# Kernel optimization log

Hardware: AMD Instinct MI355X
Metric: run time of the kernel (lower is better)

## Reference

```python
import jax, jax.numpy as jnp
import numpy as np


def _edge_softmax_by_src(e, src, n_nodes):
    # DGL edge_softmax(norm_by='src'): softmax over outgoing edges of each src node
    m = jax.ops.segment_max(e, src, num_segments=n_nodes)
    ex = jnp.exp(e - m[src])
    s = jax.ops.segment_sum(ex, src, num_segments=n_nodes)
    return ex / s[src]


def _l2norm(x):
    # F.normalize(p=2, dim=-1), eps=1e-12
    n = jnp.linalg.norm(x, axis=-1, keepdims=True)
    return x / jnp.maximum(n, 1e-12)


def setup_inputs() -> dict:
    key = jax.random.key(0)
    ks = jax.random.split(key, 16)
    N, E, D, NC = 50000, 1600000, 64, 16   # main graph nodes/edges, dim, classes
    NCL, ECL, FCL = 32, 1024, 16           # coarsened line graph: nodes=etypes
    s = 0.1
    inp = {
        "cl_h": jax.random.normal(ks[0], (NCL, FCL), jnp.float32),
        "cl_w": jax.random.normal(ks[1], (ECL,), jnp.float32),
        "cl_src": jax.random.randint(ks[2], (ECL,), 0, NCL, jnp.int32),
        "cl_dst": jax.random.randint(ks[3], (ECL,), 0, NCL, jnp.int32),
        "g_src": jax.random.randint(ks[4], (E,), 0, N, jnp.int32),
        "g_dst": jax.random.randint(ks[5], (E,), 0, N, jnp.int32),
        "g_etype": jax.random.randint(ks[6], (E,), 0, NCL, jnp.int32),
        # learned parameters
        "feats_emb": jax.random.normal(ks[7], (N, D), jnp.float32) * s,
        "W_e": jax.random.normal(ks[8], (FCL, D), jnp.float32) * s,      # linear_e (no bias)
        "beta1": jnp.array(1.0, jnp.float32),
        "eps1": jnp.array(0.0, jnp.float32),
        "beta2": jnp.array(1.0, jnp.float32),
        "eps2": jnp.array(0.0, jnp.float32),
        "W1a": jax.random.normal(ks[9], (D, D), jnp.float32) * s,
        "W2a": jax.random.normal(ks[10], (D, D), jnp.float32) * s,
        "W1b": jax.random.normal(ks[11], (D, D), jnp.float32) * s,
        "W2b": jax.random.normal(ks[12], (D, D), jnp.float32) * s,
        "W_pred": jax.random.normal(ks[13], (D, NC), jnp.float32) * s,
        "b_pred": jnp.zeros((NC,), jnp.float32),
    }
    return inp


def reference(cl_h, cl_w, cl_src, cl_dst, g_src, g_dst, g_etype,
              feats_emb, W_e, beta1, eps1, beta2, eps2,
              W1a, W2a, W1b, W2b, W_pred, b_pred):
    NCL = cl_h.shape[0]
    N = feats_emb.shape[0]

    def agnn(feat, beta, eps):
        p = _edge_softmax_by_src(beta * cl_w, cl_src, NCL)           # [Ecl]
        nh = _l2norm(feat)                                           # [NCL, F]
        agg = jax.ops.segment_sum(nh[cl_src] * p[:, None], cl_dst,
                                  num_segments=NCL)                  # [NCL, F]
        return (1.0 + eps) * feat + agg

    # edge-type feature propagation on coarsened line graph (dropout is eval-mode identity)
    h = jax.nn.relu(agnn(cl_h, beta1, eps1))
    h = jax.nn.relu(agnn(h, beta2, eps2))

    # per-edge relation embedding on main graph
    ew = h[g_etype] @ W_e                                            # [E, D]

    def gconv(feat, W1, W2):
        msg = feat[g_src] - ew                                       # u_sub_e, [E, D]
        agg = jax.ops.segment_sum(msg, g_dst, num_segments=N)        # [N, D]
        return jnp.tanh(feat @ W1 + agg @ W2)

    x = gconv(feats_emb, W1a, W2a)
    x = gconv(x, W1b, W2b)
    return x @ W_pred + b_pred
```

## Files before the change

### kernel.cpp

```cpp
#include <hip/hip_runtime.h>


#define TILE 8192

typedef __attribute__((ext_vector_type(8))) unsigned short us8;

__device__ __forceinline__ float b2f(unsigned short h) {
    return __uint_as_float(((unsigned)h) << 16);
}
__device__ __forceinline__ unsigned short f2b(float f) {
    const unsigned u = __float_as_uint(f);
    return (unsigned short)((u + 0x7FFFu + ((u >> 16) & 1u)) >> 16);
}

__device__ __forceinline__ unsigned ford_enc(float v) {
    unsigned b = __float_as_uint(v);
    return (b & 0x80000000u) ? ~b : (b | 0x80000000u);
}
__device__ __forceinline__ float ford_dec(unsigned k) {
    return __uint_as_float((k & 0x80000000u) ? (k ^ 0x80000000u) : ~k);
}

__global__ __launch_bounds__(512) void agnn_kernel(
    const float* __restrict__ cl_h, const float* __restrict__ cl_w,
    const int* __restrict__ cl_src, const int* __restrict__ cl_dst,
    const float* __restrict__ W_e,
    const float* __restrict__ pb1, const float* __restrict__ pe1,
    const float* __restrict__ pb2, const float* __restrict__ pe2,
    float* __restrict__ hW, int ECL)
{
    __shared__ float w_s[1024];
    __shared__ int   src_s[1024];
    __shared__ int   dst_s[1024];
    __shared__ float h[32][16];
    __shared__ float nh[32][16];
    __shared__ float p[1024];
    __shared__ float red[32][16];
    __shared__ float acc16[32][16][16];
    __shared__ unsigned mI[32];
    __shared__ float m[32], ssum[32], nrm[32];
    const int tid = threadIdx.x;
    const int seg = tid >> 4, j = tid & 15;

    for (int e = tid; e < ECL; e += 512) {
        w_s[e] = cl_w[e]; src_s[e] = cl_src[e]; dst_s[e] = cl_dst[e];
    }
    h[tid >> 4][tid & 15] = cl_h[tid];
    __syncthreads();

    for (int layer = 0; layer < 2; ++layer) {
        const float beta = layer ? *pb2 : *pb1;
        const float eps  = layer ? *pe2 : *pe1;

        if (tid < 32) mI[tid] = ford_enc(-3.4e38f);
        __syncthreads();
        for (int e = tid; e < ECL; e += 512)
            atomicMax(&mI[src_s[e]], ford_enc(beta * w_s[e]));
        __syncthreads();
        if (tid < 32) m[tid] = ford_dec(mI[tid]);
        __syncthreads();

        for (int e = tid; e < ECL; e += 512)
            p[e] = __expf(beta * w_s[e] - m[src_s[e]]);
        __syncthreads();

        {
            float s = 0.f;
            #pragma unroll 4
            for (int e = j; e < ECL; e += 16)
                s += (src_s[e] == seg) ? p[e] : 0.f;
            red[seg][j] = s;
        }
        __syncthreads();
        if (tid < 32) {
            float s = 0.f;
            #pragma unroll
            for (int k = 0; k < 16; ++k) s += red[tid][k];
            ssum[tid] = s;
            float q = 0.f;
            #pragma unroll
            for (int f = 0; f < 16; ++f) { float v = h[tid][f]; q += v * v; }
            nrm[tid] = fmaxf(sqrtf(q), 1e-12f);
        }
        __syncthreads();
        for (int e = tid; e < ECL; e += 512)
            p[e] = p[e] / ssum[src_s[e]];
        nh[tid >> 4][tid & 15] = h[tid >> 4][tid & 15] / nrm[tid >> 4];
        __syncthreads();

        {
            float facc[16];
            #pragma unroll
            for (int f = 0; f < 16; ++f) facc[f] = 0.f;
            #pragma unroll 4
            for (int e = j; e < ECL; e += 16) {
                if (dst_s[e] == seg) {
                    const float pe = p[e];
                    const float4* nhrow = reinterpret_cast<const float4*>(&nh[src_s[e]][0]);
                    const float4 a0 = nhrow[0], a1 = nhrow[1], a2 = nhrow[2], a3 = nhrow[3];
                    facc[0] += pe * a0.x; facc[1] += pe * a0.y; facc[2] += pe * a0.z; facc[3] += pe * a0.w;
                    facc[4] += pe * a1.x; facc[5] += pe * a1.y; facc[6] += pe * a1.z; facc[7] += pe * a1.w;
                    facc[8] += pe * a2.x; facc[9] += pe * a2.y; facc[10] += pe * a2.z; facc[11] += pe * a2.w;
                    facc[12] += pe * a3.x; facc[13] += pe * a3.y; facc[14] += pe * a3.z; facc[15] += pe * a3.w;
                }
            }
            #pragma unroll
            for (int f = 0; f < 16; ++f) acc16[seg][j][f] = facc[f];
        }
        __syncthreads();
        {
            const int t = tid >> 4, f = tid & 15;
            float a = 0.f;
            #pragma unroll
            for (int k = 0; k < 16; ++k) a += acc16[t][k][f];
            float v = (1.f + eps) * h[t][f] + a;
            h[t][f] = fmaxf(v, 0.f);
        }
        __syncthreads();
    }

    for (int o = tid; o < 2048; o += 512) {
        const int t = o >> 6, d = o & 63;
        float s = 0.f;
        #pragma unroll
        for (int f = 0; f < 16; ++f) s += h[t][f] * W_e[f * 64 + d];
        hW[o] = s;
    }
}

__global__ __launch_bounds__(256) void tobf16_kernel(
    const float* __restrict__ x, unsigned short* __restrict__ y, int total8)
{
    const int i = blockIdx.x * 256 + threadIdx.x;
    if (i >= total8) return;
    const int base = i * 8;
    const float4 a = *reinterpret_cast<const float4*>(&x[base]);
    const float4 b = *reinterpret_cast<const float4*>(&x[base + 4]);
    us8 o;
    o[0] = f2b(a.x); o[1] = f2b(a.y); o[2] = f2b(a.z); o[3] = f2b(a.w);
    o[4] = f2b(b.x); o[5] = f2b(b.y); o[6] = f2b(b.z); o[7] = f2b(b.w);
    *reinterpret_cast<us8*>(&y[base]) = o;
}

__global__ __launch_bounds__(256) void bucket_count(
    const int* __restrict__ dst, int* __restrict__ bcnt, int E)
{
    __shared__ int lh[256];
    const int tid = threadIdx.x;
    lh[tid] = 0;
    __syncthreads();
    const int base = blockIdx.x * TILE;
    #pragma unroll
    for (int it = 0; it < 8; ++it) {
        const int i = base + (it * 256 + tid) * 4;
        if (i + 3 < E) {
            const int4 d = *reinterpret_cast<const int4*>(&dst[i]);
            atomicAdd(&lh[d.x >> 8], 1); atomicAdd(&lh[d.y >> 8], 1);
            atomicAdd(&lh[d.z >> 8], 1); atomicAdd(&lh[d.w >> 8], 1);
        } else {
            for (int k = i; k < E && k < i + 4; ++k) atomicAdd(&lh[dst[k] >> 8], 1);
        }
    }
    __syncthreads();
    if (lh[tid]) atomicAdd(&bcnt[tid], lh[tid]);
}

__global__ __launch_bounds__(256) void bucket_scan(
    const int* __restrict__ bcnt, int* __restrict__ bbase, int* __restrict__ bcur)
{
    __shared__ int ws[4];
    const int tid = threadIdx.x, lane = tid & 63, wv = tid >> 6;
    const int v = bcnt[tid];
    int x = v;
    #pragma unroll
    for (int s = 1; s < 64; s <<= 1) { const int t = __shfl_up(x, s, 64); if (lane >= s) x += t; }
    if (lane == 63) ws[wv] = x;
    __syncthreads();
    if (tid == 0) { int a = ws[0]; ws[0] = 0; for (int k = 1; k < 4; ++k) { const int b = ws[k]; ws[k] = a; a += b; } }
    __syncthreads();
    const int excl = ws[wv] + x - v;
    bbase[tid] = excl; bcur[tid] = excl;
    if (tid == 255) bbase[256] = excl + v;
}

__global__ __launch_bounds__(256) void bucket_scatter(
    const int* __restrict__ src, const int* __restrict__ dst, const int* __restrict__ et,
    int* __restrict__ bcur, unsigned* __restrict__ etmp, int E)
{
    __shared__ int lh[256], lofs[256], lcur[256], gbase[256];
    __shared__ int ws[4];
    __shared__ unsigned stage[TILE];
    __shared__ unsigned char sbk[TILE];
    const int tid = threadIdx.x, lane = tid & 63, wv = tid >> 6;
    lh[tid] = 0;
    __syncthreads();
    const int base = blockIdx.x * TILE;
    #pragma unroll
    for (int it = 0; it < 8; ++it) {
        const int i = base + (it * 256 + tid) * 4;
        if (i + 3 < E) {
            const int4 d = *reinterpret_cast<const int4*>(&dst[i]);
            atomicAdd(&lh[d.x >> 8], 1); atomicAdd(&lh[d.y >> 8], 1);
            atomicAdd(&lh[d.z >> 8], 1); atomicAdd(&lh[d.w >> 8], 1);
        } else {
            for (int k = i; k < E && k < i + 4; ++k) atomicAdd(&lh[dst[k] >> 8], 1);
        }
    }
    __syncthreads();
    {
        const int v = lh[tid];
        int x = v;
        #pragma unroll
        for (int s = 1; s < 64; s <<= 1) { const int t = __shfl_up(x, s, 64); if (lane >= s) x += t; }
        if (lane == 63) ws[wv] = x;
        __syncthreads();
        if (tid == 0) { int a = ws[0]; ws[0] = 0; for (int k = 1; k < 4; ++k) { const int b = ws[k]; ws[k] = a; a += b; } }
        __syncthreads();
        const int excl = ws[wv] + x - v;
        lofs[tid] = excl; lcur[tid] = excl;
        if (v) gbase[tid] = atomicAdd(&bcur[tid], v);
    }
    __syncthreads();
    #pragma unroll
    for (int it = 0; it < 8; ++it) {
        const int i = base + (it * 256 + tid) * 4;
        if (i + 3 < E) {
            const int4 d  = *reinterpret_cast<const int4*>(&dst[i]);
            const int4 s4 = *reinterpret_cast<const int4*>(&src[i]);
            const int4 t4 = *reinterpret_cast<const int4*>(&et[i]);
            int b, r;
            b = d.x >> 8; r = atomicAdd(&lcur[b], 1);
            stage[r] = (unsigned)s4.x | ((unsigned)(d.x & 255) << 16) | ((unsigned)t4.x << 24); sbk[r] = (unsigned char)b;
            b = d.y >> 8; r = atomicAdd(&lcur[b], 1);
            stage[r] = (unsigned)s4.y | ((unsigned)(d.y & 255) << 16) | ((unsigned)t4.y << 24); sbk[r] = (unsigned char)b;
            b = d.z >> 8; r = atomicAdd(&lcur[b], 1);
            stage[r] = (unsigned)s4.z | ((unsigned)(d.z & 255) << 16) | ((unsigned)t4.z << 24); sbk[r] = (unsigned char)b;
            b = d.w >> 8; r = atomicAdd(&lcur[b], 1);
            stage[r] = (unsigned)s4.w | ((unsigned)(d.w & 255) << 16) | ((unsigned)t4.w << 24); sbk[r] = (unsigned char)b;
        } else {
            for (int k = i; k < E && k < i + 4; ++k) {
                const int b = dst[k] >> 8;
                const int r = atomicAdd(&lcur[b], 1);
                stage[r] = (unsigned)src[k] | ((unsigned)(dst[k] & 255) << 16) | ((unsigned)et[k] << 24);
                sbk[r] = (unsigned char)b;
            }
        }
    }
    __syncthreads();
    const int tot = lofs[255] + lh[255];
    for (int i = tid; i < tot; i += 256) {
        const int b = sbk[i];
        etmp[gbase[b] + (i - lofs[b])] = stage[i];
    }
}

__global__ __launch_bounds__(256) void csr_kernel(
    const unsigned* __restrict__ etmp, const int* __restrict__ bbase,
    int* __restrict__ off, unsigned* __restrict__ ssrc, int N, int NB)
{
    __shared__ int lh[256], lofs[256], lcur[256];
    __shared__ int ws[4];
    const int tid = threadIdx.x, lane = tid & 63, wv = tid >> 6;
    const int b = blockIdx.x;
    const int s = bbase[b], e = bbase[b + 1];
    lh[tid] = 0;
    __syncthreads();
    for (int i = s + tid; i < e; i += 256)
        atomicAdd(&lh[(etmp[i] >> 16) & 255], 1);
    __syncthreads();
    {
        const int v = lh[tid];
        int x = v;
        #pragma unroll
        for (int ss = 1; ss < 64; ss <<= 1) { const int t = __shfl_up(x, ss, 64); if (lane >= ss) x += t; }
        if (lane == 63) ws[wv] = x;
        __syncthreads();
        if (tid == 0) { int a = ws[0]; ws[0] = 0; for (int k = 1; k < 4; ++k) { const int c = ws[k]; ws[k] = a; a += c; } }
        __syncthreads();
        const int excl = ws[wv] + x - v;
        lofs[tid] = excl; lcur[tid] = excl;
    }
    __syncthreads();
    const int n0 = b << 8;
    if (n0 + tid < N) off[n0 + tid] = s + lofs[tid];
    if (b == NB - 1 && tid == 0) off[N] = e;
    for (int i = s + tid; i < e; i += 256) {
        const unsigned pp = etmp[i];
        const int dl = (pp >> 16) & 255;
        const int r = atomicAdd(&lcur[dl], 1);
        ssrc[s + r] = pp;
    }
}

__global__ __launch_bounds__(256) void spmm_kernel(
    const unsigned short* __restrict__ fb, const float* __restrict__ hW,
    const int* __restrict__ off, const unsigned* __restrict__ ssrc,
    float* __restrict__ aggF, int N)
{
    __shared__ float hWl[2048];
    for (int i = threadIdx.x; i < 2048; i += 256) hWl[i] = hW[i];
    __syncthreads();
    const int lane = threadIdx.x & 63;
    const int n = blockIdx.x * 4 + (threadIdx.x >> 6);
    if (n >= N) return;
    const int half = lane >> 5, c = lane & 31;
    const int beg = off[n], end = off[n + 1];
    float a0 = 0.f, a1 = 0.f;
    int i = beg + half;
    for (; i + 6 < end; i += 8) {
        unsigned pp[4];
        #pragma unroll
        for (int jj = 0; jj < 4; ++jj) pp[jj] = ssrc[i + 2 * jj];
        #pragma unroll
        for (int jj = 0; jj < 4; ++jj) {
            const unsigned u = *reinterpret_cast<const unsigned*>(
                &fb[(size_t)(pp[jj] & 0xFFFFu) * 64 + 2 * c]);
            a0 += b2f((unsigned short)(u & 0xFFFFu));
            a1 += b2f((unsigned short)(u >> 16));
        }
        #pragma unroll
        for (int jj = 0; jj < 4; ++jj) {
            const float2 hw = *reinterpret_cast<const float2*>(
                &hWl[(pp[jj] >> 24) * 64 + 2 * c]);
            a0 -= hw.x; a1 -= hw.y;
        }
    }
    for (; i < end; i += 2) {
        const unsigned pp = ssrc[i];
        const unsigned u = *reinterpret_cast<const unsigned*>(
            &fb[(size_t)(pp & 0xFFFFu) * 64 + 2 * c]);
        const float2 hw = *reinterpret_cast<const float2*>(
            &hWl[(pp >> 24) * 64 + 2 * c]);
        a0 += b2f((unsigned short)(u & 0xFFFFu)) - hw.x;
        a1 += b2f((unsigned short)(u >> 16)) - hw.y;
    }
    a0 += __shfl_xor(a0, 32);
    a1 += __shfl_xor(a1, 32);
    if (half == 0)
        *reinterpret_cast<float2*>(&aggF[(size_t)n * 64 + 2 * c]) = make_float2(a0, a1);
}

__global__ __launch_bounds__(256) void gconv_kernel(
    const float* __restrict__ Xf, const float* __restrict__ Af,
    const float* __restrict__ W1, const float* __restrict__ W2,
    float* __restrict__ x1f, unsigned short* __restrict__ out16,
    float* __restrict__ outf,
    int N, int final_mode, const float* __restrict__ Wp, const float* __restrict__ bp)
{
    __shared__ float fa[64 * 128];
    __shared__ float Wl[128 * 64];
    const int tid = threadIdx.x;
    const int nl = tid >> 2, sub = tid & 3;
    const int n0 = blockIdx.x * 64;
    const int n = n0 + nl;

    {
        const float4* w1v = reinterpret_cast<const float4*>(W1);
        const float4* w2v = reinterpret_cast<const float4*>(W2);
        float4* wlv = reinterpret_cast<float4*>(Wl);
        #pragma unroll
        for (int q = 0; q < 8; ++q) {
            const int idx = q * 256 + tid;
            wlv[idx] = (idx < 1024) ? w1v[idx] : w2v[idx - 1024];
        }
    }
    {
        float4* fav = reinterpret_cast<float4*>(fa);
        const float4* xv = reinterpret_cast<const float4*>(Xf);
        const float4* av = reinterpret_cast<const float4*>(Af);
        #pragma unroll
        for (int q = 0; q < 8; ++q) {
            const int cch = q * 256 + tid;
            const int row = cch >> 5, p = cch & 31;
            const int rn = n0 + row;
            float4 v = make_float4(0.f, 0.f, 0.f, 0.f);
            if (rn < N)
                v = (p < 16) ? xv[(size_t)rn * 16 + p] : av[(size_t)rn * 16 + (p - 16)];
            fav[row * 32 + (p ^ ((row & 7) << 2))] = v;
        }
    }
    __syncthreads();

    float acc[16];
    #pragma unroll
    for (int d = 0; d < 16; ++d) acc[d] = 0.f;

    const int swz = (nl & 7) << 2;
    const float* farow = &fa[nl * 128];
    for (int k8 = 0; k8 < 16; ++k8) {
        const int c4 = (2 * k8) ^ swz;
        const float4 f0 = *reinterpret_cast<const float4*>(&farow[c4 * 4]);
        const float4 f1 = *reinterpret_cast<const float4*>(&farow[c4 * 4 + 4]);
        const float fv[8] = {f0.x, f0.y, f0.z, f0.w, f1.x, f1.y, f1.z, f1.w};
        #pragma unroll
        for (int j = 0; j < 8; ++j) {
            const float fval = fv[j];
            const float* wrow = &Wl[(k8 * 8 + j) * 64 + sub * 16];
            #pragma unroll
            for (int d4 = 0; d4 < 4; ++d4) {
                const float4 w = *reinterpret_cast<const float4*>(&wrow[d4 * 4]);
                acc[d4 * 4 + 0] += fval * w.x;
                acc[d4 * 4 + 1] += fval * w.y;
                acc[d4 * 4 + 2] += fval * w.z;
                acc[d4 * 4 + 3] += fval * w.w;
            }
        }
    }

    #pragma unroll
    for (int d = 0; d < 16; ++d) {
        const float e2 = __expf(2.f * acc[d]);
        acc[d] = 1.f - 2.f / (e2 + 1.f);
    }

    if (!final_mode) {
        if (n < N) {
            #pragma unroll
            for (int d4 = 0; d4 < 4; ++d4) {
                const float4 v = make_float4(acc[d4 * 4], acc[d4 * 4 + 1],
                                             acc[d4 * 4 + 2], acc[d4 * 4 + 3]);
                *reinterpret_cast<float4*>(&x1f[(size_t)n * 64 + sub * 16 + d4 * 4]) = v;
            }
            us8 o0, o1;
            #pragma unroll
            for (int d = 0; d < 8; ++d) { o0[d] = f2b(acc[d]); o1[d] = f2b(acc[8 + d]); }
            *reinterpret_cast<us8*>(&out16[(size_t)n * 64 + sub * 16]) = o0;
            *reinterpret_cast<us8*>(&out16[(size_t)n * 64 + sub * 16 + 8]) = o1;
        }
    } else {
        float o[16];
        #pragma unroll
        for (int c = 0; c < 16; ++c) o[c] = 0.f;
        #pragma unroll
        for (int dd = 0; dd < 16; ++dd) {
            const float t = acc[dd];
            const float* wp = &Wp[(sub * 16 + dd) * 16];
            #pragma unroll
            for (int c4 = 0; c4 < 4; ++c4) {
                const float4 w = *reinterpret_cast<const float4*>(&wp[c4 * 4]);
                o[c4 * 4 + 0] += t * w.x;
                o[c4 * 4 + 1] += t * w.y;
                o[c4 * 4 + 2] += t * w.z;
                o[c4 * 4 + 3] += t * w.w;
            }
        }
        #pragma unroll
        for (int c = 0; c < 16; ++c) {
            o[c] += __shfl_xor(o[c], 1);
            o[c] += __shfl_xor(o[c], 2);
        }
        if (sub == 0 && n < N) {
            #pragma unroll
            for (int c = 0; c < 16; ++c) o[c] += bp[c];
            #pragma unroll
            for (int c4 = 0; c4 < 4; ++c4) {
                const float4 v = make_float4(o[c4 * 4], o[c4 * 4 + 1],
                                             o[c4 * 4 + 2], o[c4 * 4 + 3]);
                *reinterpret_cast<float4*>(&outf[(size_t)n * 16 + c4 * 4]) = v;
            }
        }
    }
}

extern "C" void kernel_launch(void* const* d_in, const int* in_sizes, int n_in,
                              void* d_out, int out_size, void* d_ws, size_t ws_size,
                              hipStream_t stream)
{
    const float* cl_h   = (const float*)d_in[0];
    const float* cl_w   = (const float*)d_in[1];
    const int*   cl_src = (const int*)d_in[2];
    const int*   cl_dst = (const int*)d_in[3];
    const int*   g_src  = (const int*)d_in[4];
    const int*   g_dst  = (const int*)d_in[5];
    const int*   g_et   = (const int*)d_in[6];
    const float* feats  = (const float*)d_in[7];
    const float* W_e    = (const float*)d_in[8];
    const float* b1     = (const float*)d_in[9];
    const float* e1     = (const float*)d_in[10];
    const float* b2     = (const float*)d_in[11];
    const float* e2     = (const float*)d_in[12];
    const float* W1a    = (const float*)d_in[13];
    const float* W2a    = (const float*)d_in[14];
    const float* W1b    = (const float*)d_in[15];
    const float* W2b    = (const float*)d_in[16];
    const float* Wp     = (const float*)d_in[17];
    const float* bp     = (const float*)d_in[18];
    const int ECL = in_sizes[1];
    const int E   = in_sizes[4];
    const int N   = in_sizes[7] / 64;
    const int NB  = (N + 255) >> 8;

    char* w = (char*)d_ws;
    auto carve = [&](size_t bytes) {
        char* r = w;
        w += (bytes + 255) & ~(size_t)255;
        return r;
    };
    float*          hW    = (float*)carve(32 * 64 * sizeof(float));
    int*            off   = (int*)carve((size_t)(N + 1) * sizeof(int));
    int*            bcnt  = (int*)carve(256 * sizeof(int));
    int*            bbase = (int*)carve(257 * sizeof(int));
    int*            bcur  = (int*)carve(256 * sizeof(int));
    unsigned*       etmp  = (unsigned*)carve((size_t)E * sizeof(unsigned));
    unsigned*       ssrc  = (unsigned*)carve((size_t)E * sizeof(unsigned));
    unsigned short* fb16  = (unsigned short*)carve((size_t)N * 64 * sizeof(unsigned short));
    unsigned short* x16   = (unsigned short*)carve((size_t)N * 64 * sizeof(unsigned short));
    float*          aggF  = (float*)carve((size_t)N * 64 * sizeof(float));
    float*          x1f   = (float*)carve((size_t)N * 64 * sizeof(float));

    const int nblk = (E + TILE - 1) / TILE;
    const int total8 = N * 8;

    hipMemsetAsync(bcnt, 0, 256 * sizeof(int), stream);

    agnn_kernel<<<1, 512, 0, stream>>>(cl_h, cl_w, cl_src, cl_dst, W_e,
                                       b1, e1, b2, e2, hW, ECL);
    tobf16_kernel<<<(total8 + 255) / 256, 256, 0, stream>>>(feats, fb16, total8);
    bucket_count<<<nblk, 256, 0, stream>>>(g_dst, bcnt, E);
    bucket_scan<<<1, 256, 0, stream>>>(bcnt, bbase, bcur);
    bucket_scatter<<<nblk, 256, 0, stream>>>(g_src, g_dst, g_et, bcur, etmp, E);
    csr_kernel<<<NB, 256, 0, stream>>>(etmp, bbase, off, ssrc, N, NB);
    spmm_kernel<<<(N + 3) / 4, 256, 0, stream>>>(fb16, hW, off, ssrc, aggF, N);
    gconv_kernel<<<(N + 63) / 64, 256, 0, stream>>>(feats, aggF, W1a, W2a,
                                                    x1f, x16, nullptr, N, 0, Wp, bp);
    spmm_kernel<<<(N + 3) / 4, 256, 0, stream>>>(x16, hW, off, ssrc, aggF, N);
    gconv_kernel<<<(N + 63) / 64, 256, 0, stream>>>(x1f, aggF, W1b, W2b,
                                                    nullptr, nullptr, (float*)d_out, N, 1, Wp, bp);
}
```

Before: 257.8 us.

## Restructure gconv dense matmul to lane-per-output-column with broadcast node rows

The node-update GEMM is reorganized so each lane owns one output column and holds a 32-wide slice of the transposed weights in registers. Node feature rows are then read directly from global memory as wave-uniform broadcast loads instead of being staged through a swizzled shared-memory tile. The final projection goes through a padded shared transpose, with each wave computing four classes for 64 nodes. This removes the shared staging of the activation tile and the shuffle reductions, at the cost of scalar per-lane stores and repeated global loads of each node row across four K chunks.

```diff
diff --git a/kernel.cpp b/kernel.cpp
--- a/kernel.cpp
+++ b/kernel.cpp
@@ -344,121 +344,90 @@
     const float* __restrict__ Xf, const float* __restrict__ Af,
     const float* __restrict__ W1, const float* __restrict__ W2,
     float* __restrict__ x1f, unsigned short* __restrict__ out16,
-    float* __restrict__ outf,
-    int N, int final_mode, const float* __restrict__ Wp, const float* __restrict__ bp)
-{
-    __shared__ float fa[64 * 128];
-    __shared__ float Wl[128 * 64];
+    float* __restrict__ outf, int N, int final_mode,
+    const float* __restrict__ Wp, const float* __restrict__ bp)
+{
+    __shared__ float WT[64 * 129];
+    __shared__ float TL[64 * 65];
     const int tid = threadIdx.x;
-    const int nl = tid >> 2, sub = tid & 3;
+    const int lane = tid & 63;
+    const int w = __builtin_amdgcn_readfirstlane(tid >> 6);
     const int n0 = blockIdx.x * 64;
-    const int n = n0 + nl;
-
-    {
-        const float4* w1v = reinterpret_cast<const float4*>(W1);
-        const float4* w2v = reinterpret_cast<const float4*>(W2);
-        float4* wlv = reinterpret_cast<float4*>(Wl);
-        #pragma unroll
-        for (int q = 0; q < 8; ++q) {
-            const int idx = q * 256 + tid;
-            wlv[idx] = (idx < 1024) ? w1v[idx] : w2v[idx - 1024];
-        }
-    }
-    {
-        float4* fav = reinterpret_cast<float4*>(fa);
-        const float4* xv = reinterpret_cast<const float4*>(Xf);
-        const float4* av = reinterpret_cast<const float4*>(Af);
-        #pragma unroll
-        for (int q = 0; q < 8; ++q) {
-            const int cch = q * 256 + tid;
-            const int row = cch >> 5, p = cch & 31;
-            const int rn = n0 + row;
-            float4 v = make_float4(0.f, 0.f, 0.f, 0.f);
-            if (rn < N)
-                v = (p < 16) ? xv[(size_t)rn * 16 + p] : av[(size_t)rn * 16 + (p - 16)];
-            fav[row * 32 + (p ^ ((row & 7) << 2))] = v;
-        }
+
+    #pragma unroll
+    for (int q = 0; q < 8; ++q) {
+        const int c = q * 256 + tid;
+        const int k = c >> 4, o4 = (c & 15) * 4;
+        const float4 v = (k < 64)
+            ? *reinterpret_cast<const float4*>(&W1[k * 64 + o4])
+            : *reinterpret_cast<const float4*>(&W2[(k - 64) * 64 + o4]);
+        WT[(o4 + 0) * 129 + k] = v.x;
+        WT[(o4 + 1) * 129 + k] = v.y;
+        WT[(o4 + 2) * 129 + k] = v.z;
+        WT[(o4 + 3) * 129 + k] = v.w;
     }
     __syncthreads();
 
     float acc[16];
     #pragma unroll
-    for (int d = 0; d < 16; ++d) acc[d] = 0.f;
-
-    const int swz = (nl & 7) << 2;
-    const float* farow = &fa[nl * 128];
-    for (int k8 = 0; k8 < 16; ++k8) {
-        const int c4 = (2 * k8) ^ swz;
-        const float4 f0 = *reinterpret_cast<const float4*>(&farow[c4 * 4]);
-        const float4 f1 = *reinterpret_cast<const float4*>(&farow[c4 * 4 + 4]);
-        const float fv[8] = {f0.x, f0.y, f0.z, f0.w, f1.x, f1.y, f1.z, f1.w};
-        #pragma unroll
-        for (int j = 0; j < 8; ++j) {
-            const float fval = fv[j];
-            const float* wrow = &Wl[(k8 * 8 + j) * 64 + sub * 16];
-            #pragma unroll
-            for (int d4 = 0; d4 < 4; ++d4) {
-                const float4 w = *reinterpret_cast<const float4*>(&wrow[d4 * 4]);
-                acc[d4 * 4 + 0] += fval * w.x;
-                acc[d4 * 4 + 1] += fval * w.y;
-                acc[d4 * 4 + 2] += fval * w.z;
-                acc[d4 * 4 + 3] += fval * w.w;
+    for (int i = 0; i < 16; ++i) acc[i] = 0.f;
+
+    for (int kc = 0; kc < 4; ++kc) {
+        float wv[32];
+        #pragma unroll
+        for (int j = 0; j < 32; ++j) wv[j] = WT[lane * 129 + kc * 32 + j];
+        #pragma unroll 4
+        for (int i = 0; i < 16; ++i) {
+            const int node = n0 + w * 16 + i;
+            if (node < N) {
+                const float* __restrict__ arow =
+                    (kc < 2) ? (Xf + (size_t)node * 64 + kc * 32)
+                             : (Af + (size_t)node * 64 + (kc - 2) * 32);
+                float s = acc[i];
+                #pragma unroll
+                for (int j4 = 0; j4 < 8; ++j4) {
+                    const float4 a = *reinterpret_cast<const float4*>(&arow[j4 * 4]);
+                    s += a.x * wv[j4 * 4 + 0];
+                    s += a.y * wv[j4 * 4 + 1];
+                    s += a.z * wv[j4 * 4 + 2];
+                    s += a.w * wv[j4 * 4 + 3];
+                }
+                acc[i] = s;
             }
         }
     }
 
     #pragma unroll
-    for (int d = 0; d < 16; ++d) {
-        const float e2 = __expf(2.f * acc[d]);
-        acc[d] = 1.f - 2.f / (e2 + 1.f);
+    for (int i = 0; i < 16; ++i) {
+        const float e2 = __expf(2.f * acc[i]);
+        acc[i] = 1.f - 2.f / (e2 + 1.f);
     }
 
     if (!final_mode) {
-        if (n < N) {
-            #pragma unroll
-            for (int d4 = 0; d4 < 4; ++d4) {
-                const float4 v = make_float4(acc[d4 * 4], acc[d4 * 4 + 1],
-                                             acc[d4 * 4 + 2], acc[d4 * 4 + 3]);
-                *reinterpret_cast<float4*>(&x1f[(size_t)n * 64 + sub * 16 + d4 * 4]) = v;
+        #pragma unroll
+        for (int i = 0; i < 16; ++i) {
+            const int node = n0 + w * 16 + i;
+            if (node < N) {
+                x1f[(size_t)node * 64 + lane] = acc[i];
+                out16[(size_t)node * 64 + lane] = f2b(acc[i]);
             }
-            us8 o0, o1;
-            #pragma unroll
-            for (int d = 0; d < 8; ++d) { o0[d] = f2b(acc[d]); o1[d] = f2b(acc[8 + d]); }
-            *reinterpret_cast<us8*>(&out16[(size_t)n * 64 + sub * 16]) = o0;
-            *reinterpret_cast<us8*>(&out16[(size_t)n * 64 + sub * 16 + 8]) = o1;
         }
     } else {
-        float o[16];
-        #pragma unroll
-        for (int c = 0; c < 16; ++c) o[c] = 0.f;
-        #pragma unroll
-        for (int dd = 0; dd < 16; ++dd) {
-            const float t = acc[dd];
-            const float* wp = &Wp[(sub * 16 + dd) * 16];
-            #pragma unroll
-            for (int c4 = 0; c4 < 4; ++c4) {
-                const float4 w = *reinterpret_cast<const float4*>(&wp[c4 * 4]);
-                o[c4 * 4 + 0] += t * w.x;
-                o[c4 * 4 + 1] += t * w.y;
-                o[c4 * 4 + 2] += t * w.z;
-                o[c4 * 4 + 3] += t * w.w;
-            }
-        }
-        #pragma unroll
-        for (int c = 0; c < 16; ++c) {
-            o[c] += __shfl_xor(o[c], 1);
-            o[c] += __shfl_xor(o[c], 2);
-        }
-        if (sub == 0 && n < N) {
-            #pragma unroll
-            for (int c = 0; c < 16; ++c) o[c] += bp[c];
-            #pragma unroll
-            for (int c4 = 0; c4 < 4; ++c4) {
-                const float4 v = make_float4(o[c4 * 4], o[c4 * 4 + 1],
-                                             o[c4 * 4 + 2], o[c4 * 4 + 3]);
-                *reinterpret_cast<float4*>(&outf[(size_t)n * 16 + c4 * 4]) = v;
-            }
-        }
+        #pragma unroll
+        for (int i = 0; i < 16; ++i)
+            TL[(w * 16 + i) * 65 + lane] = acc[i];
+        __syncthreads();
+        const int cg = w * 4;
+        float o0 = bp[cg], o1 = bp[cg + 1], o2 = bp[cg + 2], o3 = bp[cg + 3];
+        for (int d = 0; d < 64; ++d) {
+            const float tv = TL[lane * 65 + d];
+            const float4 wp = *reinterpret_cast<const float4*>(&Wp[d * 16 + cg]);
+            o0 += tv * wp.x; o1 += tv * wp.y; o2 += tv * wp.z; o3 += tv * wp.w;
+        }
+        const int node = n0 + lane;
+        if (node < N)
+            *reinterpret_cast<float4*>(&outf[(size_t)node * 16 + cg]) =
+                make_float4(o0, o1, o2, o3);
     }
 }
 
```

New measurement: 291.8 us. 1.13x slower.
